# Optimization experiments

Hardware: AMD Instinct MI355X
Metric: run time of the kernel (lower is better)

Reference implementation:

```python
import jax, jax.numpy as jnp
import numpy as np

V = 28   # len(string.ascii_lowercase + ' #')
D = 32   # embed dim
H = 2    # heads
DH = D // H
B = 64
S = 1024


def _pe(seq_len, d):
    pos = np.arange(seq_len, dtype=np.float32)[:, None]
    div = np.exp(np.arange(0, d, 2, dtype=np.float32) * (-np.log(10000.0) / d))
    pe = np.zeros((seq_len, d), np.float32)
    pe[:, 0::2] = np.sin(pos * div)
    pe[:, 1::2] = np.cos(pos * div)
    return jnp.asarray(pe)


def setup_inputs() -> dict:
    key = jax.random.key(0)
    ks = jax.random.split(key, 12)
    x = jax.random.randint(ks[0], (B, S), 0, V)
    # per-row valid length in [1, S-4] so last 1-index + 3 stays in range (as original assumes)
    lengths = jax.random.randint(ks[1], (B,), 1, S - 3)
    mask = (jnp.arange(S)[None, :] < lengths[:, None]).astype(jnp.float32)[..., None]
    sc = 1.0 / np.sqrt(D)
    emb = jax.random.normal(ks[2], (V, D), jnp.float32)
    wq = jax.random.normal(ks[3], (D, D), jnp.float32) * sc
    wk = jax.random.normal(ks[4], (D, D), jnp.float32) * sc
    wv = jax.random.normal(ks[5], (D, D), jnp.float32) * sc
    bq = jnp.zeros((D,), jnp.float32)
    bk = jnp.zeros((D,), jnp.float32)
    bv = jnp.zeros((D,), jnp.float32)
    wo = jax.random.normal(ks[6], (D, D), jnp.float32) * sc
    bo = jnp.zeros((D,), jnp.float32)
    w_fc = jax.random.normal(ks[7], (V, D), jnp.float32) * sc
    b_fc = jnp.zeros((V,), jnp.float32)
    pe = _pe(S, D)
    return {"x": x, "mask": mask, "emb": emb, "pe": pe,
            "wq": wq, "bq": bq, "wk": wk, "bk": bk, "wv": wv, "bv": bv,
            "wo": wo, "bo": bo, "w_fc": w_fc, "b_fc": b_fc}


def reference(x, mask, emb, pe, wq, bq, wk, bk, wv, bv, wo, bo, w_fc, b_fc):
    Bn, Sn = x.shape
    h = emb[x] + pe[:Sn]                      # [B,S,D]
    m = mask[..., 0]                          # [B,S]
    # vectorized "last valid index" (replaces per-row python loop + .item())
    valid = m > 0
    last = Sn - 1 - jnp.argmax(valid[:, ::-1], axis=1)   # [B]
    pos = jnp.arange(Sn)
    ext = (pos[None, :] > last[:, None]) & (pos[None, :] <= last[:, None] + 3) \
          & (last[:, None] < Sn - 1)
    nm = jnp.where(ext, jnp.float32(1.0), m)  # extended mask [B,S]
    h = h * nm[..., None]
    # multihead self-attention (torch MultiheadAttention, batch_first)
    def heads(t):
        return t.reshape(Bn, Sn, H, DH).transpose(0, 2, 1, 3)  # [B,H,S,DH]
    q = heads(h @ wq.T + bq)
    k = heads(h @ wk.T + bk)
    v = heads(h @ wv.T + bv)
    scores = jnp.einsum('bhqd,bhkd->bhqk', q, k) / jnp.sqrt(jnp.float32(DH))
    scores = jnp.where((nm == 0)[:, None, None, :], jnp.float32(-1e9), scores)
    a = jax.nn.softmax(scores, axis=-1)
    o = jnp.einsum('bhqk,bhkd->bhqd', a, v).transpose(0, 2, 1, 3).reshape(Bn, Sn, D)
    o = o @ wo.T + bo
    return o @ w_fc.T + b_fc                  # [B,S,V]
```

## Files before the change

kernel.cpp:

```cpp
#include <hip/hip_runtime.h>
#include <math.h>

#define BB 64
#define SS 1024
#define DD 32
#define HH 2
#define DHH 16
#define VV 28
#define QSC 0.3606737602222409f

typedef __attribute__((ext_vector_type(8))) short bf16x8;
typedef __attribute__((ext_vector_type(4))) float f32x4;

__device__ __forceinline__ unsigned pack_hi2(float a, float b) {
    return __builtin_amdgcn_perm(__float_as_uint(b), __float_as_uint(a), 0x07060302u);
}
__device__ __forceinline__ float trunc_hi(float a) {
    return __uint_as_float(__float_as_uint(a) & 0xFFFF0000u);
}
__device__ __forceinline__ unsigned bf_rtne_u(float x) {
    unsigned u = __float_as_uint(x);
    return (u + 0x7FFFu + ((u >> 16) & 1u)) >> 16;
}
__device__ __forceinline__ unsigned pack_rtne2(float a, float b) {
    return bf_rtne_u(a) | (bf_rtne_u(b) << 16);
}
__device__ __forceinline__ bf16x8 as_bf16x8(uint4 u) {
    union { uint4 u; bf16x8 v; } cv; cv.u = u; return cv.v;
}


__global__ __launch_bounds__(256) void k_pre(
        const int* __restrict__ x, const float* __restrict__ mask,
        const float* __restrict__ emb, const float* __restrict__ pe,
        const float* __restrict__ wq, const float* __restrict__ bq,
        const float* __restrict__ wk, const float* __restrict__ bk,
        const float* __restrict__ wv, const float* __restrict__ bv,
        const float* __restrict__ wo, const float* __restrict__ bo,
        const float* __restrict__ wfc, const float* __restrict__ bfc,
        int* __restrict__ e, float* __restrict__ W2, float* __restrict__ b2,
        char* __restrict__ qf, char* __restrict__ kf, char* __restrict__ vf) {
    int bid = blockIdx.x;
    int tid = threadIdx.x;
    if (bid < 1024) {
        __shared__ __align__(16) char hbuf[10240];
        __shared__ __align__(16) float Cb[4][16 * 17];
        char* hHi = hbuf;
        char* hLo = hbuf + 5120;
        int wave = tid >> 6, lane = tid & 63;
        int c = lane & 15, kq = lane >> 4;
        {
            int tt = tid >> 2, q4 = tid & 3;
            int idx = bid * 64 + tt;
            int b = idx >> 10, s = idx & 1023;
            float nm = (mask[b * SS + (s >= 3 ? s - 3 : 0)] != 0.0f) ? 1.0f : 0.0f;
            int tok = x[idx];
            float h[8];
#pragma unroll
            for (int i = 0; i < 8; i++)
                h[i] = (emb[tok * DD + q4 * 8 + i] + pe[s * DD + q4 * 8 + i]) * nm;
            unsigned wh[4], wl[4];
#pragma unroll
            for (int wd = 0; wd < 4; wd++) {
                float a0 = h[2 * wd], a1 = h[2 * wd + 1];
                wh[wd] = pack_hi2(a0, a1);
                wl[wd] = pack_hi2(a0 - trunc_hi(a0), a1 - trunc_hi(a1));
            }
            *(uint4*)(hHi + tt * 80 + q4 * 16) = uint4{wh[0], wh[1], wh[2], wh[3]};
            *(uint4*)(hLo + tt * 80 + q4 * 16) = uint4{wl[0], wl[1], wl[2], wl[3]};
        }
        __syncthreads();
        bf16x8 aHh, aHl;
        {
            int off = (wave * 16 + c) * 80 + kq * 16;
            aHh = *(const bf16x8*)(hHi + off);
            aHl = *(const bf16x8*)(hLo + off);
        }
        int blk_b = bid >> 4;
        int s_w = ((bid * 64) & 1023) + wave * 16;
        const f32x4 z4 = {0.0f, 0.0f, 0.0f, 0.0f};
#pragma unroll
        for (int M = 0; M < 3; M++) {
            const float* W    = M == 0 ? wq : (M == 1 ? wk : wv);
            const float* bias = M == 0 ? bq : (M == 1 ? bk : bv);
            bf16x8 Bh[2], Bl[2];
            float bv_[2];
#pragma unroll
            for (int nt = 0; nt < 2; nt++) {
                const float* wrow = W + (nt * 16 + c) * DD + kq * 8;
                float4 wa = ((const float4*)wrow)[0];
                float4 wb = ((const float4*)wrow)[1];
                float f[8] = {wa.x, wa.y, wa.z, wa.w, wb.x, wb.y, wb.z, wb.w};
                unsigned uh[4], ul[4];
#pragma unroll
                for (int wd = 0; wd < 4; wd++) {
                    float a0 = f[2 * wd], a1 = f[2 * wd + 1];
                    uh[wd] = pack_hi2(a0, a1);
                    ul[wd] = pack_hi2(a0 - trunc_hi(a0), a1 - trunc_hi(a1));
                }
                Bh[nt] = as_bf16x8(uint4{uh[0], uh[1], uh[2], uh[3]});
                Bl[nt] = as_bf16x8(uint4{ul[0], ul[1], ul[2], ul[3]});
                bv_[nt] = bias[nt * 16 + c];
            }
#pragma unroll
            for (int nt = 0; nt < 2; nt++) {
                f32x4 acc = __builtin_amdgcn_mfma_f32_16x16x32_bf16(aHh, Bh[nt], z4, 0, 0, 0);
                acc = __builtin_amdgcn_mfma_f32_16x16x32_bf16(aHl, Bh[nt], acc, 0, 0, 0);
                acc = __builtin_amdgcn_mfma_f32_16x16x32_bf16(aHh, Bl[nt], acc, 0, 0, 0);
#pragma unroll
                for (int r = 0; r < 4; r++) {
                    float val = acc[r] + bv_[nt];
                    if (M == 0) val *= QSC;
                    Cb[wave][(kq * 4 + r) * 17 + c] = val;
                }
                int bh = blk_b * 2 + nt;
                if (M == 0) {
                    int tile = s_w >> 4;
                    int qd = lane >> 4, cc = lane & 15;
                    float f[8];
#pragma unroll
                    for (int j = 0; j < 8; j++) f[j] = Cb[wave][cc * 17 + (qd & 1) * 8 + j];
                    unsigned u[4];
                    if (qd < 2) {
#pragma unroll
                        for (int wd = 0; wd < 4; wd++) u[wd] = pack_hi2(f[2 * wd], f[2 * wd + 1]);
                    } else {
#pragma unroll
                        for (int wd = 0; wd < 4; wd++) {
                            float a0 = f[2 * wd] - trunc_hi(f[2 * wd]);
                            float a1 = f[2 * wd + 1] - trunc_hi(f[2 * wd + 1]);
                            u[wd] = pack_hi2(a0, a1);
                        }
                    }
                    *(uint4*)(qf + ((size_t)((bh << 6) + tile) << 10) + lane * 16)
                        = uint4{u[0], u[1], u[2], u[3]};
                } else if (M == 1) {
                    int cl = lane & 3, qd = (lane >> 2) & 3, t = lane >> 4;
                    int ch = s_w >> 7, g1 = (s_w >> 6) & 1, c0 = (s_w & 63) >> 2;
                    int keyl = 4 * cl + t;
                    float f[8];
#pragma unroll
                    for (int j = 0; j < 8; j++) f[j] = Cb[wave][keyl * 17 + (qd & 1) * 8 + j];
                    unsigned uh[4];
#pragma unroll
                    for (int wd = 0; wd < 4; wd++) uh[wd] = pack_rtne2(f[2 * wd], f[2 * wd + 1]);
                    char* base = kf + ((size_t)((bh << 3) + ch) << 13)
                               + ((g1 << 2) + t) * 1024 + qd * 256 + (c0 + cl) * 16;
                    *(uint4*)(base) = uint4{uh[0], uh[1], uh[2], uh[3]};
                } else if (lane < 32) {
                    int gg = (s_w >> 6) & 15, Qs = (s_w >> 4) & 3;
                    int qrel = lane >> 4, dh = lane & 15;
                    unsigned u[4];
#pragma unroll
                    for (int wd = 0; wd < 4; wd++) {
                        float f0 = Cb[wave][(qrel * 8 + 2 * wd) * 17 + dh];
                        float f1 = Cb[wave][(qrel * 8 + 2 * wd + 1) * 17 + dh];
                        u[wd] = pack_rtne2(f0, f1);
                    }
                    *(uint4*)(vf + ((size_t)((bh << 5) + (gg << 1) + qrel) << 10)
                              + (Qs * 16 + dh) * 16)
                        = uint4{u[0], u[1], u[2], u[3]};
                }
            }
        }
    } else if (bid < 1088) {
        int b = bid - 1024;
        int lm = -1;
        for (int s = tid; s < SS; s += 256)
            if (mask[b * SS + s] != 0.0f) lm = s;
        __shared__ int red[256];
        red[tid] = lm;
        __syncthreads();
        for (int off = 128; off > 0; off >>= 1) {
            if (tid < off) red[tid] = max(red[tid], red[tid + off]);
            __syncthreads();
        }
        if (tid == 0) {
            int last = red[0];
            int ee = last;
            if (last < SS - 1) ee = min(last + 3, SS - 1);
            e[b] = ee;
        }
    } else {
        for (int t2 = tid; t2 < VV * DD + VV; t2 += 256) {
            if (t2 < VV * DD) {
                int vv = t2 / DD, i = t2 % DD;
                float a = 0.0f;
                for (int j = 0; j < DD; j++) a += wfc[vv * DD + j] * wo[j * DD + i];
                W2[t2] = a;
            } else {
                int vv = t2 - VV * DD;
                float a = bfc[vv];
                for (int j = 0; j < DD; j++) a += wfc[vv * DD + j] * bo[j];
                b2[vv] = a;
            }
        }
    }
}


#define LOADK(P0, P1, P2, P3, GN) {                                                \
    int gg_ = (GN) < ng ? (GN) : ng - 1;                                           \
    const char* kg_ = kbase + (size_t)gg_ * 4096;                                  \
    P0 = *(const bf16x8*)(kg_ + lane * 16);                                        \
    P1 = *(const bf16x8*)(kg_ + 1024 + lane * 16);                                 \
    P2 = *(const bf16x8*)(kg_ + 2048 + lane * 16);                                 \
    P3 = *(const bf16x8*)(kg_ + 3072 + lane * 16);                                 \
}

#define STEP(K0, K1, K2, K3, G) {                                                  \
    const char* vg_ = vbase + (size_t)(G) * 2048;                                  \
    bf16x8 v0_ = *(const bf16x8*)(vg_ + lane * 16);                                \
    bf16x8 v1_ = *(const bf16x8*)(vg_ + 1024 + lane * 16);                         \
    f32x4 st[4];                                                                   \
    st[0] = __builtin_amdgcn_mfma_f32_16x16x32_bf16(K0, aQ, z4, 0, 0, 0);          \
    st[1] = __builtin_amdgcn_mfma_f32_16x16x32_bf16(K1, aQ, z4, 0, 0, 0);          \
    st[2] = __builtin_amdgcn_mfma_f32_16x16x32_bf16(K2, aQ, z4, 0, 0, 0);          \
    st[3] = __builtin_amdgcn_mfma_f32_16x16x32_bf16(K3, aQ, z4, 0, 0, 0);          \
    if ((((G) + 1) << 6) > kmax) {                                                 \
        int kb = ((G) << 6) + (quad << 4);                                         \
        _Pragma("unroll")                                                          \
        for (int t = 0; t < 4; t++)                                                \
            _Pragma("unroll")                                                      \
            for (int r = 0; r < 4; r++)                                            \
                if (kb + 4 * r + t >= kmax) st[t][r] = -3e38f;                     \
    }                                                                              \
    float p[4][4];                                                                 \
    _Pragma("unroll")                                                              \
    for (int t = 0; t < 4; t++)                                                    \
        _Pragma("unroll")                                                          \
        for (int r = 0; r < 4; r++) p[t][r] = __builtin_amdgcn_exp2f(st[t][r]);    \
    _Pragma("unroll")                                                              \
    for (int t = 0; t < 4; t++)                                                    \
        l_ += (p[t][0] + p[t][1]) + (p[t][2] + p[t][3]);                           \
    bf16x8 pa0 = as_bf16x8(uint4{pack_hi2(p[0][0], p[1][0]), pack_hi2(p[2][0], p[3][0]), \
                                 pack_hi2(p[0][1], p[1][1]), pack_hi2(p[2][1], p[3][1])}); \
    bf16x8 pa1 = as_bf16x8(uint4{pack_hi2(p[0][2], p[1][2]), pack_hi2(p[2][2], p[3][2]), \
                                 pack_hi2(p[0][3], p[1][3]), pack_hi2(p[2][3], p[3][3])}); \
    accO = __builtin_amdgcn_mfma_f32_16x16x32_bf16(pa0, v0_, accO, 0, 0, 0);       \
    accO = __builtin_amdgcn_mfma_f32_16x16x32_bf16(pa1, v1_, accO, 0, 0, 0);       \
}

__global__ __launch_bounds__(256) void k_attn_fc(
        const char* __restrict__ qf, const char* __restrict__ kf,
        const char* __restrict__ vf, const int* __restrict__ e,
        const float* __restrict__ W2, const float* __restrict__ b2,
        float* __restrict__ out) {
    __shared__ __align__(16) float Ob[32 * 36];
    __shared__ __align__(16) float sW[VV * 36];
    __shared__ float sb[VV];
    __shared__ int skey[64];
    __shared__ int smap;
    int tid = threadIdx.x;
    int qt = blockIdx.x;

    for (int i = tid; i < VV * DD; i += 256) sW[(i >> 5) * 36 + (i & 31)] = W2[i];
    if (tid < VV) sb[tid] = b2[tid];
    if (tid < 64) skey[tid] = ((((e[tid] + 64) >> 6)) << 6) | (63 - tid);
    __syncthreads();
    if (tid < 64) {
        int mykey = skey[tid];
        int cnt = 0;
#pragma unroll
        for (int i = 0; i < 64; i++) cnt += (skey[i] > mykey) ? 1 : 0;
        if (cnt == (int)blockIdx.y) smap = tid;
    }
    __syncthreads();
    int b = smap;

    int kmax = e[b] + 1;
    int ng = (kmax + 63) >> 6;

    int wave = tid >> 6, lane = tid & 63, quad = lane >> 4, c = lane & 15;
    int h = wave & 1, ts = wave >> 1;
    int tile = (qt << 1) + ts;
    int bh = b * 2 + h;

    const char* kbase = kf + ((size_t)(bh << 3) << 13);
    const char* vbase = vf + ((size_t)bh << 15);

    bf16x8 aQ = *(const bf16x8*)(qf + ((size_t)((bh << 6) + tile) << 10) + lane * 16);
    const f32x4 z4 = {0.0f, 0.0f, 0.0f, 0.0f};
    f32x4 accO = z4;
    float l_ = 0.0f;

    bf16x8 Ak0, Ak1, Ak2, Ak3, Bk0, Bk1, Bk2, Bk3;
    LOADK(Ak0, Ak1, Ak2, Ak3, 0);
    int g = 0;
    for (; g + 2 <= ng; g += 2) {
        LOADK(Bk0, Bk1, Bk2, Bk3, g + 1);
        STEP(Ak0, Ak1, Ak2, Ak3, g);
        LOADK(Ak0, Ak1, Ak2, Ak3, g + 2);
        STEP(Bk0, Bk1, Bk2, Bk3, g + 1);
    }
    if (g < ng) { STEP(Ak0, Ak1, Ak2, Ak3, g); }

    l_ += __shfl_xor(l_, 16);
    l_ += __shfl_xor(l_, 32);

    float* obr = Ob + (ts * 16 + quad * 4) * 36 + h * 16 + c;
#pragma unroll
    for (int r = 0; r < 4; r++) {
        float lr = __shfl(l_, (quad << 2) + r, 16);
        obr[r * 36] = accO[r] * __builtin_amdgcn_rcpf(lr);
    }
    __syncthreads();

    int rl = tid >> 3, j = tid & 7;
    if (j < 7) {
        const float* orow = Ob + rl * 36;
        float ov[DD];
#pragma unroll
        for (int i = 0; i < DD; i += 4) {
            float4 t4 = *(const float4*)(orow + i);
            ov[i] = t4.x; ov[i + 1] = t4.y; ov[i + 2] = t4.z; ov[i + 3] = t4.w;
        }
        int v0 = j << 2;
        float res[4];
#pragma unroll
        for (int k = 0; k < 4; k++) {
            int vv = v0 + k;
            float a = sb[vv];
#pragma unroll
            for (int d = 0; d < DD; d += 4) {
                float4 w4 = *(const float4*)(sW + vv * 36 + d);
                a += ov[d] * w4.x + ov[d + 1] * w4.y + ov[d + 2] * w4.z + ov[d + 3] * w4.w;
            }
            res[k] = a;
        }
        int q = (qt << 5) + rl;
        size_t off = ((size_t)((b << 10) + q)) * VV + v0;
        *(float4*)(out + off) = float4{res[0], res[1], res[2], res[3]};
    }
}

extern "C" void kernel_launch(void* const* d_in, const int* in_sizes, int n_in,
                              void* d_out, int out_size, void* d_ws, size_t ws_size,
                              hipStream_t stream) {
    const int*   x    = (const int*)d_in[0];
    const float* mask = (const float*)d_in[1];
    const float* emb  = (const float*)d_in[2];
    const float* pe   = (const float*)d_in[3];
    const float* wq   = (const float*)d_in[4];
    const float* bq   = (const float*)d_in[5];
    const float* wk   = (const float*)d_in[6];
    const float* bk   = (const float*)d_in[7];
    const float* wv   = (const float*)d_in[8];
    const float* bv   = (const float*)d_in[9];
    const float* wo   = (const float*)d_in[10];
    const float* bo   = (const float*)d_in[11];
    const float* wfc  = (const float*)d_in[12];
    const float* bfc  = (const float*)d_in[13];
    float* out = (float*)d_out;

    char* ws = (char*)d_ws;
    int*   e  = (int*)ws;
    float* W2 = (float*)(ws + 256);
    float* b2 = (float*)(ws + 3840);
    char*  qf = ws + 4096;
    char*  kf = qf + (size_t)8388608;
    char*  vf = kf + (size_t)8388608;

    hipLaunchKernelGGL(k_pre, dim3(1089), dim3(256), 0, stream,
                       x, mask, emb, pe, wq, bq, wk, bk, wv, bv, wo, bo, wfc, bfc,
                       e, W2, b2, qf, kf, vf);
    hipLaunchKernelGGL(k_attn_fc, dim3(SS / 32, BB), dim3(256), 0, stream,
                       qf, kf, vf, e, W2, b2, out);
}
```

Baseline: 120.1 us.

## Split attention key range across waves with split-K merge through shared memory

Result: slower. 129.4 us (+7.8%).

```diff
diff --git a/kernel.cpp b/kernel.cpp
--- a/kernel.cpp
+++ b/kernel.cpp
@@ -200,7 +200,7 @@
 
 
 #define LOADK(P0, P1, P2, P3, GN) {                                                \
-    int gg_ = (GN) < ng ? (GN) : ng - 1;                                           \
+    int gg_ = (GN) < ge ? (GN) : ge - 1;                                           \
     const char* kg_ = kbase + (size_t)gg_ * 4096;                                  \
     P0 = *(const bf16x8*)(kg_ + lane * 16);                                        \
     P1 = *(const bf16x8*)(kg_ + 1024 + lane * 16);                                 \
@@ -246,9 +246,11 @@
         const char* __restrict__ vf, const int* __restrict__ e,
         const float* __restrict__ W2, const float* __restrict__ b2,
         float* __restrict__ out) {
-    __shared__ __align__(16) float Ob[32 * 36];
+    __shared__ __align__(16) float Ob[16 * 36];
     __shared__ __align__(16) float sW[VV * 36];
     __shared__ float sb[VV];
+    __shared__ __align__(16) float accP[4][64][4];
+    __shared__ float lP[4][64];
     __shared__ int skey[64];
     __shared__ int smap;
     int tid = threadIdx.x;
@@ -270,43 +272,55 @@
 
     int kmax = e[b] + 1;
     int ng = (kmax + 63) >> 6;
+    int nga = (ng + 1) >> 1;
 
     int wave = tid >> 6, lane = tid & 63, quad = lane >> 4, c = lane & 15;
-    int h = wave & 1, ts = wave >> 1;
-    int tile = (qt << 1) + ts;
+    int h = wave & 1, chunk = wave >> 1;
+    int gb = chunk ? nga : 0;
+    int ge = chunk ? ng : nga;
     int bh = b * 2 + h;
 
     const char* kbase = kf + ((size_t)(bh << 3) << 13);
     const char* vbase = vf + ((size_t)bh << 15);
 
-    bf16x8 aQ = *(const bf16x8*)(qf + ((size_t)((bh << 6) + tile) << 10) + lane * 16);
+    bf16x8 aQ = *(const bf16x8*)(qf + ((size_t)((bh << 6) + qt) << 10) + lane * 16);
     const f32x4 z4 = {0.0f, 0.0f, 0.0f, 0.0f};
     f32x4 accO = z4;
     float l_ = 0.0f;
 
-    bf16x8 Ak0, Ak1, Ak2, Ak3, Bk0, Bk1, Bk2, Bk3;
-    LOADK(Ak0, Ak1, Ak2, Ak3, 0);
-    int g = 0;
-    for (; g + 2 <= ng; g += 2) {
-        LOADK(Bk0, Bk1, Bk2, Bk3, g + 1);
-        STEP(Ak0, Ak1, Ak2, Ak3, g);
-        LOADK(Ak0, Ak1, Ak2, Ak3, g + 2);
-        STEP(Bk0, Bk1, Bk2, Bk3, g + 1);
-    }
-    if (g < ng) { STEP(Ak0, Ak1, Ak2, Ak3, g); }
+    if (gb < ge) {
+        bf16x8 Ak0, Ak1, Ak2, Ak3, Bk0, Bk1, Bk2, Bk3;
+        LOADK(Ak0, Ak1, Ak2, Ak3, gb);
+        int g = gb;
+        for (; g + 2 <= ge; g += 2) {
+            LOADK(Bk0, Bk1, Bk2, Bk3, g + 1);
+            STEP(Ak0, Ak1, Ak2, Ak3, g);
+            LOADK(Ak0, Ak1, Ak2, Ak3, g + 2);
+            STEP(Bk0, Bk1, Bk2, Bk3, g + 1);
+        }
+        if (g < ge) { STEP(Ak0, Ak1, Ak2, Ak3, g); }
+    }
 
     l_ += __shfl_xor(l_, 16);
     l_ += __shfl_xor(l_, 32);
 
-    float* obr = Ob + (ts * 16 + quad * 4) * 36 + h * 16 + c;
-#pragma unroll
-    for (int r = 0; r < 4; r++) {
-        float lr = __shfl(l_, (quad << 2) + r, 16);
-        obr[r * 36] = accO[r] * __builtin_amdgcn_rcpf(lr);
-    }
+    *(f32x4*)&accP[wave][lane][0] = accO;
+    lP[wave][lane] = l_;
     __syncthreads();
 
-    int rl = tid >> 3, j = tid & 7;
+    if (wave < 2) {
+        f32x4 po = *(const f32x4*)&accP[wave + 2][lane][0];
+        float lf = l_ + lP[wave + 2][lane];
+        float* obr = Ob + (quad * 4) * 36 + (h << 4) + c;
+#pragma unroll
+        for (int r = 0; r < 4; r++) {
+            float lr = __shfl(lf, (quad << 2) + r, 16);
+            obr[r * 36] = (accO[r] + po[r]) * __builtin_amdgcn_rcpf(lr);
+        }
+    }
+    __syncthreads();
+
+    int rl = tid >> 4, j = tid & 15;
     if (j < 7) {
         const float* orow = Ob + rl * 36;
         float ov[DD];
@@ -328,7 +342,7 @@
             }
             res[k] = a;
         }
-        int q = (qt << 5) + rl;
+        int q = (qt << 4) + rl;
         size_t off = ((size_t)((b << 10) + q)) * VV + v0;
         *(float4*)(out + off) = float4{res[0], res[1], res[2], res[3]};
     }
@@ -364,6 +378,6 @@
     hipLaunchKernelGGL(k_pre, dim3(1089), dim3(256), 0, stream,
                        x, mask, emb, pe, wq, bq, wk, bk, wv, bv, wo, bo, wfc, bfc,
                        e, W2, b2, qf, kf, vf);
-    hipLaunchKernelGGL(k_attn_fc, dim3(SS / 32, BB), dim3(256), 0, stream,
+    hipLaunchKernelGGL(k_attn_fc, dim3(64, BB), dim3(256), 0, stream,
                        qf, kf, vf, e, W2, b2, out);
 }
```

## Compact K fragment layout to halve K buffer and loads

Applied to the files above, without the earlier changes.

Result: no change. 120.3 us (+0.2%).

```diff
diff --git a/kernel.cpp b/kernel.cpp
--- a/kernel.cpp
+++ b/kernel.cpp
@@ -135,18 +135,15 @@
                     *(uint4*)(qf + ((size_t)((bh << 6) + tile) << 10) + lane * 16)
                         = uint4{u[0], u[1], u[2], u[3]};
                 } else if (M == 1) {
-                    int cl = lane & 3, qd = (lane >> 2) & 3, t = lane >> 4;
-                    int ch = s_w >> 7, g1 = (s_w >> 6) & 1, c0 = (s_w & 63) >> 2;
-                    int keyl = 4 * cl + t;
-                    float f[8];
-#pragma unroll
-                    for (int j = 0; j < 8; j++) f[j] = Cb[wave][keyl * 17 + (qd & 1) * 8 + j];
-                    unsigned uh[4];
-#pragma unroll
-                    for (int wd = 0; wd < 4; wd++) uh[wd] = pack_rtne2(f[2 * wd], f[2 * wd + 1]);
-                    char* base = kf + ((size_t)((bh << 3) + ch) << 13)
-                               + ((g1 << 2) + t) * 1024 + qd * 256 + (c0 + cl) * 16;
-                    *(uint4*)(base) = uint4{uh[0], uh[1], uh[2], uh[3]};
+                    int keyl = lane >> 2, dq = lane & 3;
+                    int gg = (s_w >> 6) & 15, c0 = (s_w & 63) >> 2;
+                    float f0 = Cb[wave][keyl * 17 + dq * 4 + 0];
+                    float f1 = Cb[wave][keyl * 17 + dq * 4 + 1];
+                    float f2 = Cb[wave][keyl * 17 + dq * 4 + 2];
+                    float f3 = Cb[wave][keyl * 17 + dq * 4 + 3];
+                    *(uint2*)(kf + ((size_t)bh << 15) + gg * 2048 + (keyl & 3) * 512
+                              + (c0 + (keyl >> 2)) * 32 + dq * 8)
+                        = uint2{pack_rtne2(f0, f1), pack_rtne2(f2, f3)};
                 } else if (lane < 32) {
                     int gg = (s_w >> 6) & 15, Qs = (s_w >> 4) & 3;
                     int qrel = lane >> 4, dh = lane & 15;
@@ -201,11 +198,11 @@
 
 #define LOADK(P0, P1, P2, P3, GN) {                                                \
     int gg_ = (GN) < ng ? (GN) : ng - 1;                                           \
-    const char* kg_ = kbase + (size_t)gg_ * 4096;                                  \
-    P0 = *(const bf16x8*)(kg_ + lane * 16);                                        \
-    P1 = *(const bf16x8*)(kg_ + 1024 + lane * 16);                                 \
-    P2 = *(const bf16x8*)(kg_ + 2048 + lane * 16);                                 \
-    P3 = *(const bf16x8*)(kg_ + 3072 + lane * 16);                                 \
+    const char* kg_ = kbase + (size_t)gg_ * 2048;                                  \
+    P0 = *(const bf16x8*)(kg_ + koff);                                             \
+    P1 = *(const bf16x8*)(kg_ + 512 + koff);                                       \
+    P2 = *(const bf16x8*)(kg_ + 1024 + koff);                                      \
+    P3 = *(const bf16x8*)(kg_ + 1536 + koff);                                      \
 }
 
 #define STEP(K0, K1, K2, K3, G) {                                                  \
@@ -275,8 +272,9 @@
     int h = wave & 1, ts = wave >> 1;
     int tile = (qt << 1) + ts;
     int bh = b * 2 + h;
-
-    const char* kbase = kf + ((size_t)(bh << 3) << 13);
+    int koff = (c << 5) + ((quad & 1) << 4);
+
+    const char* kbase = kf + ((size_t)bh << 15);
     const char* vbase = vf + ((size_t)bh << 15);
 
     bf16x8 aQ = *(const bf16x8*)(qf + ((size_t)((bh << 6) + tile) << 10) + lane * 16);
@@ -359,7 +357,7 @@
     float* b2 = (float*)(ws + 3840);
     char*  qf = ws + 4096;
     char*  kf = qf + (size_t)8388608;
-    char*  vf = kf + (size_t)8388608;
+    char*  vf = kf + (size_t)4194304;
 
     hipLaunchKernelGGL(k_pre, dim3(1089), dim3(256), 0, stream,
                        x, mask, emb, pe, wq, bq, wk, bk, wv, bv, wo, bo, wfc, bfc,
```
